# Optimization experiments

Measured on AMD Instinct MI355X. Metric: run time of the kernel, lower is better.

## Reference

```python
import jax, jax.numpy as jnp
import numpy as np

NUM_HEADS = 16
EMB_DIM = 1024
IN_CH = 512
D_CTX = 768
DEPTH = EMB_DIM // NUM_HEADS
SCALE = DEPTH ** -0.5
NEG = -1e9


def setup_inputs() -> dict:
    key = jax.random.key(0)
    ks = jax.random.split(key, 12)
    B, N, S = 4, 4096, 256
    def lin(kw, fan_in, fan_out):
        lim = 1.0 / np.sqrt(fan_in)
        w = jax.random.uniform(kw, (fan_out, fan_in), jnp.float32, -lim, lim)
        return w
    return {
        'x': jax.random.normal(ks[0], (B, N, IN_CH), jnp.float32),
        'context': jax.random.normal(ks[1], (B, S, D_CTX), jnp.float32),
        'pad_mask': jnp.ones((B, N), jnp.float32),
        'seq_mask': jnp.ones((B, S), jnp.float32),
        'Wq_w': lin(ks[2], IN_CH, EMB_DIM), 'Wq_b': jnp.zeros((EMB_DIM,), jnp.float32),
        'Wk_w': lin(ks[3], D_CTX, EMB_DIM), 'Wk_b': jnp.zeros((EMB_DIM,), jnp.float32),
        'Wv_w': lin(ks[4], D_CTX, EMB_DIM), 'Wv_b': jnp.zeros((EMB_DIM,), jnp.float32),
        'P1_w': lin(ks[5], EMB_DIM, EMB_DIM), 'P1_b': jnp.zeros((EMB_DIM,), jnp.float32),
        'P2_w': lin(ks[6], EMB_DIM, IN_CH), 'P2_b': jnp.zeros((IN_CH,), jnp.float32),
    }


def reference(x, context, pad_mask, seq_mask, Wq_w, Wq_b, Wk_w, Wk_b, Wv_w, Wv_b, P1_w, P1_b, P2_w, P2_b):
    B, N, _ = x.shape
    S = context.shape[1]
    # QKV projections, split into heads: [B, H, N|S, D]
    Q = (x @ Wq_w.T + Wq_b).reshape(B, N, NUM_HEADS, DEPTH).transpose(0, 2, 1, 3)
    K = (context @ Wk_w.T + Wk_b).reshape(B, S, NUM_HEADS, DEPTH).transpose(0, 2, 1, 3)
    V = (context @ Wv_w.T + Wv_b).reshape(B, S, NUM_HEADS, DEPTH).transpose(0, 2, 1, 3)
    # attention scores [B, H, N, S]
    att = jnp.einsum('bnid,bnjd->bnij', Q, K) * SCALE
    # outer-product mask: pad_mask[B,N] x seq_mask[B,S] -> [B,1,N,S]
    mask = (pad_mask[:, :, None] * seq_mask[:, None, :])[:, None, :, :]
    att = jnp.where(mask != 0.0, att, NEG)
    att = jax.nn.softmax(att, axis=-1)
    out = jnp.einsum('bnij,bnjd->bnid', att, V)
    out = out.transpose(0, 2, 1, 3).reshape(B, N, EMB_DIM)
    # proj_out MLP: Linear -> ReLU -> Linear
    out = jax.nn.relu(out @ P1_w.T + P1_b) @ P2_w.T + P2_b
    return out
```

## Files before the change

kernel.cpp:

```cpp
#include <hip/hip_runtime.h>
#include <hip/hip_bf16.h>
#include <stdint.h>

typedef __attribute__((ext_vector_type(8))) short bf16x8;
typedef __attribute__((ext_vector_type(4))) short s16x4;
typedef __attribute__((ext_vector_type(4))) float f32x4;

#define MFMA16(a, b, c) __builtin_amdgcn_mfma_f32_16x16x32_bf16((a), (b), (c), 0, 0, 0)
#define MFMAH(a, b, c) __builtin_amdgcn_mfma_f32_16x16x16bf16_1k((a), (b), (c), 0, 0, 0)

__device__ __forceinline__ void gload_lds16(const void* g, void* l) {
  __builtin_amdgcn_global_load_lds((const __attribute__((address_space(1))) void*)g,
                                   (__attribute__((address_space(3))) void*)l, 16, 0, 0);
}

__global__ void cvt_all(const float* __restrict__ s0, const float* __restrict__ s1,
                        const float* __restrict__ s2, const float* __restrict__ s3,
                        const float* __restrict__ s4, const float* __restrict__ s5,
                        const float* __restrict__ s6,
                        __hip_bfloat16* __restrict__ d0, __hip_bfloat16* __restrict__ d1,
                        __hip_bfloat16* __restrict__ d2, __hip_bfloat16* __restrict__ d3,
                        __hip_bfloat16* __restrict__ d4, __hip_bfloat16* __restrict__ d5,
                        __hip_bfloat16* __restrict__ d6) {
  constexpr int e0 = 2097152;
  constexpr int e1 = e0 + 196608;
  constexpr int e2 = e1 + 131072;
  constexpr int e3 = e2 + 196608;
  constexpr int e4 = e3 + 196608;
  constexpr int e5 = e4 + 262144;
  constexpr int e6 = e5 + 131072;
  const int stride = gridDim.x * blockDim.x;
  for (int i = blockIdx.x * blockDim.x + threadIdx.x; i < e6; i += stride) {
    const float* s; __hip_bfloat16* d; int j;
    if (i < e0)      { s = s0; d = d0; j = i; }
    else if (i < e1) { s = s1; d = d1; j = i - e0; }
    else if (i < e2) { s = s2; d = d2; j = i - e1; }
    else if (i < e3) { s = s3; d = d3; j = i - e2; }
    else if (i < e4) { s = s4; d = d4; j = i - e3; }
    else if (i < e5) { s = s5; d = d5; j = i - e4; }
    else             { s = s6; d = d6; j = i - e5; }
    const float4 v = *(const float4*)(s + (size_t)j * 4);
    s16x4 o;
    __hip_bfloat16 h;
    h = __float2bfloat16(v.x); o[0] = *(short*)&h;
    h = __float2bfloat16(v.y); o[1] = *(short*)&h;
    h = __float2bfloat16(v.z); o[2] = *(short*)&h;
    h = __float2bfloat16(v.w); o[3] = *(short*)&h;
    *(s16x4*)((short*)d + (size_t)j * 4) = o;
  }
}


template <int RELU, int OUTMODE>
__global__ __launch_bounds__(256, 2) void gemm_bt(
    const __hip_bfloat16* __restrict__ Abf, const __hip_bfloat16* __restrict__ Wbf,
    const float* __restrict__ bias, void* __restrict__ Cv,
    int M, int N, int K) {
  __shared__ __align__(16) __hip_bfloat16 As[128 * 32];
  __shared__ __align__(16) __hip_bfloat16 Bs[128 * 32];
  const int t = threadIdx.x;
  const int w = t >> 6, lane = t & 63;
  const int lr = lane & 15, lg = lane >> 4;
  const int m0 = blockIdx.x * 128, n0 = blockIdx.y * 128;
  const int wr = (w >> 1) * 64, wc = (w & 1) * 64;

  const char* Ag = (const char*)Abf;
  const char* Wg = (const char*)Wbf;
  const size_t ldb = (size_t)K * 2;

  f32x4 acc[4][4] = {};

  const int o0 = (w << 10) + lane * 16;
  const int o1 = o0 + 4096;
  const int r0 = o0 >> 6, gc0 = ((((o0 >> 4) & 3) ^ ((r0 >> 1) & 3)) << 4);
  const int r1 = o1 >> 6, gc1 = ((((o1 >> 4) & 3) ^ ((r1 >> 1) & 3)) << 4);
  const int slx = (lg ^ ((lr >> 1) & 3)) << 4;

  for (int kt = 0; kt < K; kt += 32) {
    if (kt) __syncthreads();
    gload_lds16(Ag + (size_t)(m0 + r0) * ldb + kt * 2 + gc0, (char*)As + (w << 10));
    gload_lds16(Ag + (size_t)(m0 + r1) * ldb + kt * 2 + gc1, (char*)As + 4096 + (w << 10));
    gload_lds16(Wg + (size_t)(n0 + r0) * ldb + kt * 2 + gc0, (char*)Bs + (w << 10));
    gload_lds16(Wg + (size_t)(n0 + r1) * ldb + kt * 2 + gc1, (char*)Bs + 4096 + (w << 10));
    __syncthreads();

    bf16x8 af[4], bfv[4];
#pragma unroll
    for (int mi = 0; mi < 4; ++mi)
      af[mi] = *(const bf16x8*)((const char*)As + ((wr + mi * 16 + lr) << 6) + slx);
#pragma unroll
    for (int ni = 0; ni < 4; ++ni)
      bfv[ni] = *(const bf16x8*)((const char*)Bs + ((wc + ni * 16 + lr) << 6) + slx);
#pragma unroll
    for (int mi = 0; mi < 4; ++mi)
#pragma unroll
      for (int ni = 0; ni < 4; ++ni)
        acc[mi][ni] = MFMA16(af[mi], bfv[ni], acc[mi][ni]);
  }

#pragma unroll
  for (int ni = 0; ni < 4; ++ni) {
    const int col = n0 + wc + ni * 16 + lr;
    const float bv = bias[col];
#pragma unroll
    for (int mi = 0; mi < 4; ++mi) {
      const int row = m0 + wr + mi * 16 + lg * 4;
#pragma unroll
      for (int j = 0; j < 4; ++j) {
        float v = acc[mi][ni][j] + bv;
        if (RELU) v = fmaxf(v, 0.0f);
        if (OUTMODE == 0) {
          ((__hip_bfloat16*)Cv)[(size_t)(row + j) * N + col] = __float2bfloat16(v);
        } else if (OUTMODE == 1) {
          ((float*)Cv)[(size_t)(row + j) * N + col] = v;
        } else {
          const int rb = (row + j) >> 8, s = (row + j) & 255;
          const int hh = col >> 6, d = col & 63;
          ((__hip_bfloat16*)Cv)[(((size_t)(rb * 16 + hh) * 64 + d) << 8) + s] =
              __float2bfloat16(v);
        }
      }
    }
  }
}

__device__ __forceinline__ void gemm256_body(
    const __hip_bfloat16* __restrict__ Abf, const __hip_bfloat16* __restrict__ Wbf,
    const float* __restrict__ bias, __hip_bfloat16* __restrict__ C,
    int N, int K, int outmode, int relu, int bx, int by) {
  __shared__ __align__(16) __hip_bfloat16 AsB[4][256 * 32];
  __shared__ __align__(16) __hip_bfloat16 BsB[4][256 * 32];
  const int t = threadIdx.x;
  const int w = t >> 6, lane = t & 63;
  const int lr = lane & 15, lg = lane >> 4;
  const int m0 = bx * 256, n0 = by * 256;
  const int wr = (w >> 2) * 128, wc = (w & 3) * 64;

  const char* Ag = (const char*)Abf;
  const char* Wg = (const char*)Wbf;
  const size_t ldb = (size_t)K * 2;

  f32x4 acc[8][4] = {};

  const int o0 = (w << 10) + lane * 16;
  const int o1 = o0 + 8192;
  const int r0 = o0 >> 6, gc0 = ((((o0 >> 4) & 3) ^ ((r0 >> 1) & 3)) << 4);
  const int r1 = o1 >> 6, gc1 = ((((o1 >> 4) & 3) ^ ((r1 >> 1) & 3)) << 4);
  const int slx = (lg ^ ((lr >> 1) & 3)) << 4;
  const int db0 = (w << 10);
  const int db1 = 8192 + (w << 10);

  auto STAGE_A = [&](int buf, int tile) {
    const int kt = tile << 5;
    gload_lds16(Ag + (size_t)(m0 + r0) * ldb + kt * 2 + gc0, (char*)AsB[buf] + db0);
    gload_lds16(Ag + (size_t)(m0 + r1) * ldb + kt * 2 + gc1, (char*)AsB[buf] + db1);
  };
  auto STAGE_B = [&](int buf, int tile) {
    const int kt = tile << 5;
    gload_lds16(Wg + (size_t)(n0 + r0) * ldb + kt * 2 + gc0, (char*)BsB[buf] + db0);
    gload_lds16(Wg + (size_t)(n0 + r1) * ldb + kt * 2 + gc1, (char*)BsB[buf] + db1);
  };

  auto tile_body = [&](int j, int stage_tile, int vmsel) {
    const int buf = j & 3;
    const int nbuf = stage_tile & 3;
    bf16x8 af0[4], af1[4], bfv[4];
#pragma unroll
    for (int mi = 0; mi < 4; ++mi)
      af0[mi] = *(const bf16x8*)((const char*)AsB[buf] + ((wr + mi * 16 + lr) << 6) + slx);
#pragma unroll
    for (int ni = 0; ni < 4; ++ni)
      bfv[ni] = *(const bf16x8*)((const char*)BsB[buf] + ((wc + ni * 16 + lr) << 6) + slx);
    if (stage_tile >= 0) STAGE_A(nbuf, stage_tile);
    asm volatile("s_barrier" ::: "memory");
    asm volatile("s_waitcnt lgkmcnt(0)" ::: "memory");
    __builtin_amdgcn_sched_barrier(0);
    __builtin_amdgcn_s_setprio(1);
#pragma unroll
    for (int mi = 0; mi < 4; ++mi)
#pragma unroll
      for (int ni = 0; ni < 4; ++ni)
        acc[mi][ni] = MFMA16(af0[mi], bfv[ni], acc[mi][ni]);
    __builtin_amdgcn_s_setprio(0);
    asm volatile("s_barrier" ::: "memory");
#pragma unroll
    for (int mi = 0; mi < 4; ++mi)
      af1[mi] = *(const bf16x8*)((const char*)AsB[buf] + ((wr + (mi + 4) * 16 + lr) << 6) + slx);
    if (stage_tile >= 0) STAGE_B(nbuf, stage_tile);
    if (vmsel == 0)      asm volatile("s_waitcnt vmcnt(8)" ::: "memory");
    else if (vmsel == 1) asm volatile("s_waitcnt vmcnt(4)" ::: "memory");
    else if (vmsel == 2) asm volatile("s_waitcnt vmcnt(0)" ::: "memory");
    asm volatile("s_barrier" ::: "memory");
    asm volatile("s_waitcnt lgkmcnt(0)" ::: "memory");
    __builtin_amdgcn_sched_barrier(0);
    __builtin_amdgcn_s_setprio(1);
#pragma unroll
    for (int mi = 0; mi < 4; ++mi)
#pragma unroll
      for (int ni = 0; ni < 4; ++ni)
        acc[mi + 4][ni] = MFMA16(af1[mi], bfv[ni], acc[mi + 4][ni]);
    __builtin_amdgcn_s_setprio(0);
    asm volatile("s_barrier" ::: "memory");
  };

  const int nt = K >> 5;
  STAGE_A(0, 0); STAGE_B(0, 0);
  STAGE_A(1, 1); STAGE_B(1, 1);
  STAGE_A(2, 2); STAGE_B(2, 2);
  asm volatile("s_waitcnt vmcnt(8)" ::: "memory");
  asm volatile("s_barrier" ::: "memory");
  for (int j = 0; j < nt - 3; ++j)
    tile_body(j, j + 3, 0);
  tile_body(nt - 3, -1, 1);
  tile_body(nt - 2, -1, 2);
  tile_body(nt - 1, -1, 3);

#pragma unroll
  for (int ni = 0; ni < 4; ++ni) {
    const int col = n0 + wc + ni * 16 + lr;
    const float bv = bias[col];
#pragma unroll
    for (int mi = 0; mi < 8; ++mi) {
      const int row = m0 + wr + mi * 16 + lg * 4;
#pragma unroll
      for (int j = 0; j < 4; ++j) {
        float v = acc[mi][ni][j] + bv;
        if (relu) v = fmaxf(v, 0.0f);
        if (outmode == 0) {
          C[(size_t)(row + j) * N + col] = __float2bfloat16(v);
        } else {
          const int rb = (row + j) >> 8, s = (row + j) & 255;
          const int hh = col >> 6, d = col & 63;
          C[(((size_t)(rb * 16 + hh) * 64 + d) << 8) + s] = __float2bfloat16(v);
        }
      }
    }
  }
}

__device__ __forceinline__ void gemm256_lite(
    const __hip_bfloat16* __restrict__ Abf, const __hip_bfloat16* __restrict__ Wbf,
    const float* __restrict__ bias, __hip_bfloat16* __restrict__ C,
    int N, int K, int outmode, int relu, int bx, int by) {
  __shared__ __align__(16) __hip_bfloat16 AsL[2][256 * 32];
  __shared__ __align__(16) __hip_bfloat16 BsL[2][256 * 32];
  const int t = threadIdx.x;
  const int w = t >> 6, lane = t & 63;
  const int lr = lane & 15, lg = lane >> 4;
  const int m0 = bx * 256, n0 = by * 256;
  const int wr = (w >> 2) * 128, wc = (w & 3) * 64;

  const char* Ag = (const char*)Abf;
  const char* Wg = (const char*)Wbf;
  const size_t ldb = (size_t)K * 2;

  f32x4 acc[8][4] = {};

  const int o0 = (w << 10) + lane * 16;
  const int o1 = o0 + 8192;
  const int r0 = o0 >> 6, gc0 = ((((o0 >> 4) & 3) ^ ((r0 >> 1) & 3)) << 4);
  const int r1 = o1 >> 6, gc1 = ((((o1 >> 4) & 3) ^ ((r1 >> 1) & 3)) << 4);
  const int slx = (lg ^ ((lr >> 1) & 3)) << 4;
  const int db0 = (w << 10);
  const int db1 = 8192 + (w << 10);

  auto STAGE_A = [&](int buf, int tile) {
    const int kt = tile << 5;
    gload_lds16(Ag + (size_t)(m0 + r0) * ldb + kt * 2 + gc0, (char*)AsL[buf] + db0);
    gload_lds16(Ag + (size_t)(m0 + r1) * ldb + kt * 2 + gc1, (char*)AsL[buf] + db1);
  };
  auto STAGE_B = [&](int buf, int tile) {
    const int kt = tile << 5;
    gload_lds16(Wg + (size_t)(n0 + r0) * ldb + kt * 2 + gc0, (char*)BsL[buf] + db0);
    gload_lds16(Wg + (size_t)(n0 + r1) * ldb + kt * 2 + gc1, (char*)BsL[buf] + db1);
  };

  const int nt = K >> 5;
  STAGE_A(0, 0); STAGE_B(0, 0);
  asm volatile("s_waitcnt vmcnt(0)" ::: "memory");
  asm volatile("s_barrier" ::: "memory");
  for (int j = 0; j < nt; ++j) {
    const int buf = j & 1;
    const int stage = (j + 1 < nt);
    bf16x8 af0[4], af1[4], bfv[4];
#pragma unroll
    for (int mi = 0; mi < 4; ++mi)
      af0[mi] = *(const bf16x8*)((const char*)AsL[buf] + ((wr + mi * 16 + lr) << 6) + slx);
#pragma unroll
    for (int ni = 0; ni < 4; ++ni)
      bfv[ni] = *(const bf16x8*)((const char*)BsL[buf] + ((wc + ni * 16 + lr) << 6) + slx);
    if (stage) STAGE_A(buf ^ 1, j + 1);
    asm volatile("s_barrier" ::: "memory");
    asm volatile("s_waitcnt lgkmcnt(0)" ::: "memory");
    __builtin_amdgcn_sched_barrier(0);
    __builtin_amdgcn_s_setprio(1);
#pragma unroll
    for (int mi = 0; mi < 4; ++mi)
#pragma unroll
      for (int ni = 0; ni < 4; ++ni)
        acc[mi][ni] = MFMA16(af0[mi], bfv[ni], acc[mi][ni]);
    __builtin_amdgcn_s_setprio(0);
    asm volatile("s_barrier" ::: "memory");
#pragma unroll
    for (int mi = 0; mi < 4; ++mi)
      af1[mi] = *(const bf16x8*)((const char*)AsL[buf] + ((wr + (mi + 4) * 16 + lr) << 6) + slx);
    if (stage) STAGE_B(buf ^ 1, j + 1);
    asm volatile("s_barrier" ::: "memory");
    asm volatile("s_waitcnt lgkmcnt(0)" ::: "memory");
    __builtin_amdgcn_sched_barrier(0);
    __builtin_amdgcn_s_setprio(1);
#pragma unroll
    for (int mi = 0; mi < 4; ++mi)
#pragma unroll
      for (int ni = 0; ni < 4; ++ni)
        acc[mi + 4][ni] = MFMA16(af1[mi], bfv[ni], acc[mi + 4][ni]);
    __builtin_amdgcn_s_setprio(0);
    if (stage) asm volatile("s_waitcnt vmcnt(0)" ::: "memory");
    asm volatile("s_barrier" ::: "memory");
  }

#pragma unroll
  for (int ni = 0; ni < 4; ++ni) {
    const int col = n0 + wc + ni * 16 + lr;
    const float bv = bias[col];
#pragma unroll
    for (int mi = 0; mi < 8; ++mi) {
      const int row = m0 + wr + mi * 16 + lg * 4;
#pragma unroll
      for (int j = 0; j < 4; ++j) {
        float v = acc[mi][ni][j] + bv;
        if (relu) v = fmaxf(v, 0.0f);
        if (outmode == 0) {
          C[(size_t)(row + j) * N + col] = __float2bfloat16(v);
        } else {
          const int rb = (row + j) >> 8, s = (row + j) & 255;
          const int hh = col >> 6, d = col & 63;
          C[(((size_t)(rb * 16 + hh) * 64 + d) << 8) + s] = __float2bfloat16(v);
        }
      }
    }
  }
}

__global__ __launch_bounds__(512, 2) void gemm256_qkv(
    const __hip_bfloat16* __restrict__ xb, const __hip_bfloat16* __restrict__ ctxb,
    const __hip_bfloat16* __restrict__ Wq, const __hip_bfloat16* __restrict__ Wk,
    const __hip_bfloat16* __restrict__ Wv,
    const float* __restrict__ bq, const float* __restrict__ bk, const float* __restrict__ bv,
    __hip_bfloat16* __restrict__ Q, __hip_bfloat16* __restrict__ Kp,
    __hip_bfloat16* __restrict__ Vt) {
  const int bid = blockIdx.x;
  if (bid < 16) {
    gemm256_lite(ctxb, Wk, bk, Kp, 1024, 768, 0, 0, bid >> 2, bid & 3);
  } else if (bid < 32) {
    const int l = bid - 16;
    gemm256_lite(ctxb, Wv, bv, Vt, 1024, 768, 2, 0, l >> 2, l & 3);
  } else {
    const int l = bid - 32;
    const int rb = (l & 7) * 32 + (l >> 3);
    gemm256_lite(xb, Wq, bq, Q, 1024, 512, 0, 0, rb >> 2, rb & 3);
  }
}

__global__ __launch_bounds__(512, 2) void gemm256_p1(
    const __hip_bfloat16* __restrict__ A, const __hip_bfloat16* __restrict__ W,
    const float* __restrict__ bias, __hip_bfloat16* __restrict__ C) {
  const int bid = blockIdx.x;
  const int rb = (bid & 7) * 32 + (bid >> 3);
  gemm256_body(A, W, bias, C, 1024, 1024, 0, 1, rb >> 2, rb & 3);
}

__global__ __launch_bounds__(512, 4) void attn_fused(
    const __hip_bfloat16* __restrict__ Qb, const __hip_bfloat16* __restrict__ Kb,
    const __hip_bfloat16* __restrict__ Vtg, const float* __restrict__ padm,
    const float* __restrict__ seqm, __hip_bfloat16* __restrict__ O) {
  constexpr int S = 256, E = 1024, Nq = 4096;
  constexpr float NEGV = -1e9f;
  __shared__ __align__(16) char smem[65536];
  char* VtB = smem;
  char* KsB = smem + 32768;

  const int t = threadIdx.x;
  const int w = t >> 6, lane = t & 63;
  const int lr = lane & 15, lg = lane >> 4;
  const int h = blockIdx.y, b = blockIdx.z;

  const char* Kg = (const char*)(Kb + (size_t)b * S * E + h * 64);
#pragma unroll
  for (int i = 0; i < 4; ++i) {
    const int o = ((i * 8 + w) << 10) + lane * 16;
    const int s = o >> 7, bc = o & 127;
    gload_lds16(Kg + (size_t)s * (E * 2) + (bc ^ ((s & 7) << 4)), KsB + ((i * 8 + w) << 10));
  }
  const char* Vg = (const char*)Vtg + ((size_t)(b * 16 + h) << 15);
#pragma unroll
  for (int i = 0; i < 4; ++i) {
    const int o = ((i * 8 + w) << 10) + lane * 16;
    const int d = o >> 9, c = o & 511;
    gload_lds16(Vg + (d << 9) + (c ^ ((d & 7) << 4)), VtB + ((i * 8 + w) << 10));
  }

  const int qw = blockIdx.x * 128 + w * 16;
  const short* Qg = (const short*)Qb + (size_t)(b * Nq + qw + lr) * E + h * 64;
  const bf16x8 aq0 = *(const bf16x8*)(Qg + (lg << 3));
  const bf16x8 aq1 = *(const bf16x8*)(Qg + 32 + (lg << 3));
  const float padq = padm[(size_t)b * Nq + qw + lr];
  const float qbias = (padq != 0.f) ? 0.f : NEGV;

  __syncthreads();

  const int swz = (lr & 7) << 4;
  f32x4 o[4] = {};
  float ssum = 0.f;
#pragma unroll
  for (int ni = 0; ni < 16; ++ni) {
    const int s = ni * 16 + lr;
    const bf16x8 bk0 = *(const bf16x8*)(KsB + (s << 7) + ((lg << 4) ^ swz));
    const bf16x8 bk1 = *(const bf16x8*)(KsB + (s << 7) + ((64 + (lg << 4)) ^ swz));
    f32x4 a = {};
    a = MFMA16(bk0, aq0, a);
    a = MFMA16(bk1, aq1, a);

    const float4 sm4 = *(const float4*)(seqm + (size_t)b * S + ni * 16 + lg * 4);
    const float e0 = __expf(a[0] * 0.125f + ((sm4.x != 0.f ? 0.f : NEGV) + qbias));
    const float e1 = __expf(a[1] * 0.125f + ((sm4.y != 0.f ? 0.f : NEGV) + qbias));
    const float e2 = __expf(a[2] * 0.125f + ((sm4.z != 0.f ? 0.f : NEGV) + qbias));
    const float e3 = __expf(a[3] * 0.125f + ((sm4.w != 0.f ? 0.f : NEGV) + qbias));
    ssum += (e0 + e1) + (e2 + e3);

    s16x4 pf;
    __hip_bfloat16 hh;
    hh = __float2bfloat16(e0); pf[0] = *(short*)&hh;
    hh = __float2bfloat16(e1); pf[1] = *(short*)&hh;
    hh = __float2bfloat16(e2); pf[2] = *(short*)&hh;
    hh = __float2bfloat16(e3); pf[3] = *(short*)&hh;

    const int sb = (ni * 32 + lg * 8);
#pragma unroll
    for (int nd = 0; nd < 4; ++nd) {
      const int d = nd * 16 + lr;
      const s16x4 bv = *(const s16x4*)(VtB + (d << 9) + (sb ^ swz));
      o[nd] = MFMAH(pf, bv, o[nd]);
    }
  }

  ssum += __shfl_xor(ssum, 16);
  ssum += __shfl_xor(ssum, 32);
  const float inv = 1.0f / ssum;
  float invj[4];
#pragma unroll
  for (int j = 0; j < 4; ++j) invj[j] = __shfl(inv, lg * 4 + j);

  __hip_bfloat16* Og = O + (size_t)(b * Nq + qw) * E + h * 64;
#pragma unroll
  for (int nd = 0; nd < 4; ++nd)
#pragma unroll
    for (int j = 0; j < 4; ++j)
      Og[(size_t)(lg * 4 + j) * E + nd * 16 + lr] = __float2bfloat16(o[nd][j] * invj[j]);
}

extern "C" void kernel_launch(void* const* d_in, const int* in_sizes, int n_in,
                              void* d_out, int out_size, void* d_ws, size_t ws_size,
                              hipStream_t stream) {
  const float* x    = (const float*)d_in[0];
  const float* ctx  = (const float*)d_in[1];
  const float* padm = (const float*)d_in[2];
  const float* seqm = (const float*)d_in[3];
  const float* Wq_w = (const float*)d_in[4];
  const float* Wq_b = (const float*)d_in[5];
  const float* Wk_w = (const float*)d_in[6];
  const float* Wk_b = (const float*)d_in[7];
  const float* Wv_w = (const float*)d_in[8];
  const float* Wv_b = (const float*)d_in[9];
  const float* P1_w = (const float*)d_in[10];
  const float* P1_b = (const float*)d_in[11];
  const float* P2_w = (const float*)d_in[12];
  const float* P2_b = (const float*)d_in[13];
  float* out = (float*)d_out;

  char* ws = (char*)d_ws;
  size_t off = 0;
  auto alloc = [&](size_t bytes) { char* p = ws + off; off += (bytes + 255) & ~(size_t)255; return p; };
  __hip_bfloat16* Q    = (__hip_bfloat16*)alloc(16384ull * 1024 * 2);
  __hip_bfloat16* AO   = (__hip_bfloat16*)alloc(16384ull * 1024 * 2);
  __hip_bfloat16* xb   = (__hip_bfloat16*)alloc(16384ull * 512 * 2);
  __hip_bfloat16* ctxb = (__hip_bfloat16*)alloc(1024ull * 768 * 2);
  __hip_bfloat16* Kp   = (__hip_bfloat16*)alloc(1024ull * 1024 * 2);
  __hip_bfloat16* Vt   = (__hip_bfloat16*)alloc(1024ull * 1024 * 2);
  __hip_bfloat16* Wqb  = (__hip_bfloat16*)alloc(1024ull * 512 * 2);
  __hip_bfloat16* Wkb  = (__hip_bfloat16*)alloc(1024ull * 768 * 2);
  __hip_bfloat16* Wvb  = (__hip_bfloat16*)alloc(1024ull * 768 * 2);
  __hip_bfloat16* P1b  = (__hip_bfloat16*)alloc(1024ull * 1024 * 2);
  __hip_bfloat16* P2b  = (__hip_bfloat16*)alloc(512ull * 1024 * 2);
  __hip_bfloat16* O1   = Q;

  cvt_all<<<dim3(2048, 1, 1), dim3(256, 1, 1), 0, stream>>>(
      x, ctx, Wq_w, Wk_w, Wv_w, P1_w, P2_w, xb, ctxb, Wqb, Wkb, Wvb, P1b, P2b);

  gemm256_qkv<<<dim3(288, 1, 1), dim3(512, 1, 1), 0, stream>>>(
      xb, ctxb, Wqb, Wkb, Wvb, Wq_b, Wk_b, Wv_b, Q, Kp, Vt);
  attn_fused<<<dim3(32, 16, 4), dim3(512, 1, 1), 0, stream>>>(Q, Kp, Vt, padm, seqm, AO);
  gemm256_p1<<<dim3(256, 1, 1), dim3(512, 1, 1), 0, stream>>>(AO, P1b, P1_b, O1);
  gemm_bt<0, 1><<<dim3(128, 4, 1), dim3(256, 1, 1), 0, stream>>>(O1, P2b, P2_b, out, 16384, 512, 1024);
}
```

Baseline: 168.6 us.

## Use 128-row tiles for QKV GEMMs and double-buffered pipeline for P1

The QKV projection kernel now uses 128x256 tiles with half the accumulators, doubling its block count and raising the occupancy hint from 2 to 4 blocks per CU. The P1 GEMM switches from the 4-stage LDS pipeline to the simpler 2-stage double-buffered loop, which halves its LDS footprint but waits for all outstanding loads every k-tile. The goal is more parallelism and occupancy for the small-K GEMMs. The trade-off is less operand reuse per block and less prefetch depth to hide memory latency in P1.

```diff
diff --git a/kernel.cpp b/kernel.cpp
--- a/kernel.cpp
+++ b/kernel.cpp
@@ -124,12 +124,12 @@
   }
 }
 
-__device__ __forceinline__ void gemm256_body(
+__device__ __forceinline__ void gemm256_lite(
     const __hip_bfloat16* __restrict__ Abf, const __hip_bfloat16* __restrict__ Wbf,
     const float* __restrict__ bias, __hip_bfloat16* __restrict__ C,
     int N, int K, int outmode, int relu, int bx, int by) {
-  __shared__ __align__(16) __hip_bfloat16 AsB[4][256 * 32];
-  __shared__ __align__(16) __hip_bfloat16 BsB[4][256 * 32];
+  __shared__ __align__(16) __hip_bfloat16 AsL[2][256 * 32];
+  __shared__ __align__(16) __hip_bfloat16 BsL[2][256 * 32];
   const int t = threadIdx.x;
   const int w = t >> 6, lane = t & 63;
   const int lr = lane & 15, lg = lane >> 4;
@@ -152,26 +152,30 @@
 
   auto STAGE_A = [&](int buf, int tile) {
     const int kt = tile << 5;
-    gload_lds16(Ag + (size_t)(m0 + r0) * ldb + kt * 2 + gc0, (char*)AsB[buf] + db0);
-    gload_lds16(Ag + (size_t)(m0 + r1) * ldb + kt * 2 + gc1, (char*)AsB[buf] + db1);
+    gload_lds16(Ag + (size_t)(m0 + r0) * ldb + kt * 2 + gc0, (char*)AsL[buf] + db0);
+    gload_lds16(Ag + (size_t)(m0 + r1) * ldb + kt * 2 + gc1, (char*)AsL[buf] + db1);
   };
   auto STAGE_B = [&](int buf, int tile) {
     const int kt = tile << 5;
-    gload_lds16(Wg + (size_t)(n0 + r0) * ldb + kt * 2 + gc0, (char*)BsB[buf] + db0);
-    gload_lds16(Wg + (size_t)(n0 + r1) * ldb + kt * 2 + gc1, (char*)BsB[buf] + db1);
+    gload_lds16(Wg + (size_t)(n0 + r0) * ldb + kt * 2 + gc0, (char*)BsL[buf] + db0);
+    gload_lds16(Wg + (size_t)(n0 + r1) * ldb + kt * 2 + gc1, (char*)BsL[buf] + db1);
   };
 
-  auto tile_body = [&](int j, int stage_tile, int vmsel) {
-    const int buf = j & 3;
-    const int nbuf = stage_tile & 3;
+  const int nt = K >> 5;
+  STAGE_A(0, 0); STAGE_B(0, 0);
+  asm volatile("s_waitcnt vmcnt(0)" ::: "memory");
+  asm volatile("s_barrier" ::: "memory");
+  for (int j = 0; j < nt; ++j) {
+    const int buf = j & 1;
+    const int stage = (j + 1 < nt);
     bf16x8 af0[4], af1[4], bfv[4];
 #pragma unroll
     for (int mi = 0; mi < 4; ++mi)
-      af0[mi] = *(const bf16x8*)((const char*)AsB[buf] + ((wr + mi * 16 + lr) << 6) + slx);
+      af0[mi] = *(const bf16x8*)((const char*)AsL[buf] + ((wr + mi * 16 + lr) << 6) + slx);
 #pragma unroll
     for (int ni = 0; ni < 4; ++ni)
-      bfv[ni] = *(const bf16x8*)((const char*)BsB[buf] + ((wc + ni * 16 + lr) << 6) + slx);
-    if (stage_tile >= 0) STAGE_A(nbuf, stage_tile);
+      bfv[ni] = *(const bf16x8*)((const char*)BsL[buf] + ((wc + ni * 16 + lr) << 6) + slx);
+    if (stage) STAGE_A(buf ^ 1, j + 1);
     asm volatile("s_barrier" ::: "memory");
     asm volatile("s_waitcnt lgkmcnt(0)" ::: "memory");
     __builtin_amdgcn_sched_barrier(0);
@@ -185,11 +189,8 @@
     asm volatile("s_barrier" ::: "memory");
 #pragma unroll
     for (int mi = 0; mi < 4; ++mi)
-      af1[mi] = *(const bf16x8*)((const char*)AsB[buf] + ((wr + (mi + 4) * 16 + lr) << 6) + slx);
-    if (stage_tile >= 0) STAGE_B(nbuf, stage_tile);
-    if (vmsel == 0)      asm volatile("s_waitcnt vmcnt(8)" ::: "memory");
-    else if (vmsel == 1) asm volatile("s_waitcnt vmcnt(4)" ::: "memory");
-    else if (vmsel == 2) asm volatile("s_waitcnt vmcnt(0)" ::: "memory");
+      af1[mi] = *(const bf16x8*)((const char*)AsL[buf] + ((wr + (mi + 4) * 16 + lr) << 6) + slx);
+    if (stage) STAGE_B(buf ^ 1, j + 1);
     asm volatile("s_barrier" ::: "memory");
     asm volatile("s_waitcnt lgkmcnt(0)" ::: "memory");
     __builtin_amdgcn_sched_barrier(0);
@@ -200,20 +201,9 @@
       for (int ni = 0; ni < 4; ++ni)
         acc[mi + 4][ni] = MFMA16(af1[mi], bfv[ni], acc[mi + 4][ni]);
     __builtin_amdgcn_s_setprio(0);
-    asm volatile("s_barrier" ::: "memory");
-  };
-
-  const int nt = K >> 5;
-  STAGE_A(0, 0); STAGE_B(0, 0);
-  STAGE_A(1, 1); STAGE_B(1, 1);
-  STAGE_A(2, 2); STAGE_B(2, 2);
-  asm volatile("s_waitcnt vmcnt(8)" ::: "memory");
-  asm volatile("s_barrier" ::: "memory");
-  for (int j = 0; j < nt - 3; ++j)
-    tile_body(j, j + 3, 0);
-  tile_body(nt - 3, -1, 1);
-  tile_body(nt - 2, -1, 2);
-  tile_body(nt - 1, -1, 3);
+    if (stage) asm volatile("s_waitcnt vmcnt(0)" ::: "memory");
+    asm volatile("s_barrier" ::: "memory");
+  }
 
 #pragma unroll
   for (int ni = 0; ni < 4; ++ni) {
@@ -238,23 +228,23 @@
   }
 }
 
-__device__ __forceinline__ void gemm256_lite(
+__device__ __forceinline__ void gemm128_lite(
     const __hip_bfloat16* __restrict__ Abf, const __hip_bfloat16* __restrict__ Wbf,
     const float* __restrict__ bias, __hip_bfloat16* __restrict__ C,
     int N, int K, int outmode, int relu, int bx, int by) {
-  __shared__ __align__(16) __hip_bfloat16 AsL[2][256 * 32];
+  __shared__ __align__(16) __hip_bfloat16 AsL[2][128 * 32];
   __shared__ __align__(16) __hip_bfloat16 BsL[2][256 * 32];
   const int t = threadIdx.x;
   const int w = t >> 6, lane = t & 63;
   const int lr = lane & 15, lg = lane >> 4;
-  const int m0 = bx * 256, n0 = by * 256;
-  const int wr = (w >> 2) * 128, wc = (w & 3) * 64;
+  const int m0 = bx * 128, n0 = by * 256;
+  const int wr = (w >> 2) * 64, wc = (w & 3) * 64;
 
   const char* Ag = (const char*)Abf;
   const char* Wg = (const char*)Wbf;
   const size_t ldb = (size_t)K * 2;
 
-  f32x4 acc[8][4] = {};
+  f32x4 acc[4][4] = {};
 
   const int o0 = (w << 10) + lane * 16;
   const int o1 = o0 + 8192;
@@ -267,7 +257,6 @@
   auto STAGE_A = [&](int buf, int tile) {
     const int kt = tile << 5;
     gload_lds16(Ag + (size_t)(m0 + r0) * ldb + kt * 2 + gc0, (char*)AsL[buf] + db0);
-    gload_lds16(Ag + (size_t)(m0 + r1) * ldb + kt * 2 + gc1, (char*)AsL[buf] + db1);
   };
   auto STAGE_B = [&](int buf, int tile) {
     const int kt = tile << 5;
@@ -282,9 +271,9 @@
   for (int j = 0; j < nt; ++j) {
     const int buf = j & 1;
     const int stage = (j + 1 < nt);
-    bf16x8 af0[4], af1[4], bfv[4];
-#pragma unroll
-    for (int mi = 0; mi < 4; ++mi)
+    bf16x8 af0[2], af1[2], bfv[4];
+#pragma unroll
+    for (int mi = 0; mi < 2; ++mi)
       af0[mi] = *(const bf16x8*)((const char*)AsL[buf] + ((wr + mi * 16 + lr) << 6) + slx);
 #pragma unroll
     for (int ni = 0; ni < 4; ++ni)
@@ -295,25 +284,25 @@
     __builtin_amdgcn_sched_barrier(0);
     __builtin_amdgcn_s_setprio(1);
 #pragma unroll
-    for (int mi = 0; mi < 4; ++mi)
+    for (int mi = 0; mi < 2; ++mi)
 #pragma unroll
       for (int ni = 0; ni < 4; ++ni)
         acc[mi][ni] = MFMA16(af0[mi], bfv[ni], acc[mi][ni]);
     __builtin_amdgcn_s_setprio(0);
     asm volatile("s_barrier" ::: "memory");
 #pragma unroll
-    for (int mi = 0; mi < 4; ++mi)
-      af1[mi] = *(const bf16x8*)((const char*)AsL[buf] + ((wr + (mi + 4) * 16 + lr) << 6) + slx);
+    for (int mi = 0; mi < 2; ++mi)
+      af1[mi] = *(const bf16x8*)((const char*)AsL[buf] + ((wr + (mi + 2) * 16 + lr) << 6) + slx);
     if (stage) STAGE_B(buf ^ 1, j + 1);
     asm volatile("s_barrier" ::: "memory");
     asm volatile("s_waitcnt lgkmcnt(0)" ::: "memory");
     __builtin_amdgcn_sched_barrier(0);
     __builtin_amdgcn_s_setprio(1);
 #pragma unroll
-    for (int mi = 0; mi < 4; ++mi)
+    for (int mi = 0; mi < 2; ++mi)
 #pragma unroll
       for (int ni = 0; ni < 4; ++ni)
-        acc[mi + 4][ni] = MFMA16(af1[mi], bfv[ni], acc[mi + 4][ni]);
+        acc[mi + 2][ni] = MFMA16(af1[mi], bfv[ni], acc[mi + 2][ni]);
     __builtin_amdgcn_s_setprio(0);
     if (stage) asm volatile("s_waitcnt vmcnt(0)" ::: "memory");
     asm volatile("s_barrier" ::: "memory");
@@ -324,7 +313,7 @@
     const int col = n0 + wc + ni * 16 + lr;
     const float bv = bias[col];
 #pragma unroll
-    for (int mi = 0; mi < 8; ++mi) {
+    for (int mi = 0; mi < 4; ++mi) {
       const int row = m0 + wr + mi * 16 + lg * 4;
 #pragma unroll
       for (int j = 0; j < 4; ++j) {
@@ -342,7 +331,7 @@
   }
 }
 
-__global__ __launch_bounds__(512, 2) void gemm256_qkv(
+__global__ __launch_bounds__(512, 4) void gemm256_qkv(
     const __hip_bfloat16* __restrict__ xb, const __hip_bfloat16* __restrict__ ctxb,
     const __hip_bfloat16* __restrict__ Wq, const __hip_bfloat16* __restrict__ Wk,
     const __hip_bfloat16* __restrict__ Wv,
@@ -350,15 +339,15 @@
     __hip_bfloat16* __restrict__ Q, __hip_bfloat16* __restrict__ Kp,
     __hip_bfloat16* __restrict__ Vt) {
   const int bid = blockIdx.x;
-  if (bid < 16) {
-    gemm256_lite(ctxb, Wk, bk, Kp, 1024, 768, 0, 0, bid >> 2, bid & 3);
-  } else if (bid < 32) {
-    const int l = bid - 16;
-    gemm256_lite(ctxb, Wv, bv, Vt, 1024, 768, 2, 0, l >> 2, l & 3);
+  if (bid < 32) {
+    gemm128_lite(ctxb, Wk, bk, Kp, 1024, 768, 0, 0, bid >> 2, bid & 3);
+  } else if (bid < 64) {
+    const int l = bid - 32;
+    gemm128_lite(ctxb, Wv, bv, Vt, 1024, 768, 2, 0, l >> 2, l & 3);
   } else {
-    const int l = bid - 32;
-    const int rb = (l & 7) * 32 + (l >> 3);
-    gemm256_lite(xb, Wq, bq, Q, 1024, 512, 0, 0, rb >> 2, rb & 3);
+    const int l = bid - 64;
+    const int rb = (l & 7) * 64 + (l >> 3);
+    gemm128_lite(xb, Wq, bq, Q, 1024, 512, 0, 0, rb >> 2, rb & 3);
   }
 }
 
@@ -367,7 +356,7 @@
     const float* __restrict__ bias, __hip_bfloat16* __restrict__ C) {
   const int bid = blockIdx.x;
   const int rb = (bid & 7) * 32 + (bid >> 3);
-  gemm256_body(A, W, bias, C, 1024, 1024, 0, 1, rb >> 2, rb & 3);
+  gemm256_lite(A, W, bias, C, 1024, 1024, 0, 1, rb >> 2, rb & 3);
 }
 
 __global__ __launch_bounds__(512, 4) void attn_fused(
@@ -497,7 +486,7 @@
   cvt_all<<<dim3(2048, 1, 1), dim3(256, 1, 1), 0, stream>>>(
       x, ctx, Wq_w, Wk_w, Wv_w, P1_w, P2_w, xb, ctxb, Wqb, Wkb, Wvb, P1b, P2b);
 
-  gemm256_qkv<<<dim3(288, 1, 1), dim3(512, 1, 1), 0, stream>>>(
+  gemm256_qkv<<<dim3(576, 1, 1), dim3(512, 1, 1), 0, stream>>>(
       xb, ctxb, Wqb, Wkb, Wvb, Wq_b, Wk_b, Wv_b, Q, Kp, Vt);
   attn_fused<<<dim3(32, 16, 4), dim3(512, 1, 1), 0, stream>>>(Q, Kp, Vt, padm, seqm, AO);
   gemm256_p1<<<dim3(256, 1, 1), dim3(512, 1, 1), 0, stream>>>(AO, P1b, P1_b, O1);
```

New measurement: 156.0 us. -7.5%, faster.
